# Optimization experiments

Hardware: AMD Instinct MI355X
Metric: run time of the kernel (lower is better)

## Reference

```python
import jax, jax.numpy as jnp
import numpy as np

B, T, D, H = 4, 2048, 1024, 8
d = D // H
EPS = 1e-12  # torch F.normalize eps


def _l2norm(x):
    n = jnp.sqrt(jnp.sum(x * x, axis=-1, keepdims=True))
    return x / jnp.maximum(n, EPS)


def setup_inputs() -> dict:
    key = jax.random.key(0)
    ks = jax.random.split(key, 7)
    s = 1.0 / np.sqrt(D)
    return {
        "x": jax.random.normal(ks[0], (B, T, D), dtype=jnp.float32),
        "Wq": jax.random.uniform(ks[1], (D, D), jnp.float32, -s, s),
        "Wk": jax.random.uniform(ks[2], (D, D), jnp.float32, -s, s),
        "Wv": jax.random.uniform(ks[3], (D, D), jnp.float32, -s, s),
        "Wo": jax.random.uniform(ks[4], (D, D), jnp.float32, -s, s),
        "Wlr": jax.random.uniform(ks[5], (D, D), jnp.float32, -s, s),
        "b_lr": jnp.zeros((D,), jnp.float32),
    }


def reference(x, Wq, Wk, Wv, Wo, Wlr, b_lr):
    # projections (torch Linear: y = x @ W.T)
    q = (x @ Wq.T).reshape(B, T, H, d)
    k = _l2norm((x @ Wk.T).reshape(B, T, H, d))
    v = _l2norm((x @ Wv.T).reshape(B, T, H, d))
    lr = jax.nn.sigmoid(x @ Wlr.T + b_lr).reshape(B, T, H, d)

    # scan over time; state w: [B,H,d,d]
    def step(w, qkvl):
        q_t, k_t, v_t, lr_t = qkvl  # each [B,H,d]
        v_old = jnp.einsum('bhij,bhj->bhi', w, k_t)          # retrieve
        w = w + (lr_t * (v_t - v_old))[..., :, None] * k_t[..., None, :]
        o_t = jnp.einsum('bhij,bhj->bhi', w, q_t)            # read
        return w, o_t

    to_t = lambda a: jnp.moveaxis(a, 1, 0)  # [B,T,H,d] -> [T,B,H,d]
    w0 = jnp.zeros((B, H, d, d), dtype=q.dtype)
    _, o = jax.lax.scan(step, w0, (to_t(q), to_t(k), to_t(v), to_t(lr)))
    o = jnp.moveaxis(o, 0, 1).reshape(B, T, D)
    return o @ Wo.T
```

## Files before the change

### kernel.cpp

```cpp
#include <hip/hip_runtime.h>
#include <math.h>

#define Bsz  4
#define Tlen 2048
#define Dm   1024
#define Hh   8
#define dh   128
#define Mrows (Bsz * Tlen)
#define CH   128
#define NCH  (Tlen / CH)

typedef __attribute__((ext_vector_type(8))) short  s16x8;
typedef __attribute__((ext_vector_type(4))) float  f32x4;

#define DPP_ADD(x, ctrl) \
    ((x) + __int_as_float(__builtin_amdgcn_update_dpp( \
        0, __float_as_int(x), (ctrl), 0xf, 0xf, true)))
#define SWZ_ADD16(x) \
    ((x) + __int_as_float(__builtin_amdgcn_ds_swizzle(__float_as_int(x), 0x401F)))

__device__ inline unsigned short f2b_rne(float f) {
    unsigned int u = __float_as_uint(f);
    u += 0x7FFFu + ((u >> 16) & 1u);
    return (unsigned short)(u >> 16);
}

__global__ __launch_bounds__(256) void cvt_f32_bf16(const float* __restrict__ in,
                                                    unsigned short* __restrict__ out)
{
    const size_t i = ((size_t)blockIdx.x * 256 + threadIdx.x) * 4;
    float4 v = *(const float4*)&in[i];
    ushort4 o;
    o.x = f2b_rne(v.x); o.y = f2b_rne(v.y);
    o.z = f2b_rne(v.z); o.w = f2b_rne(v.w);
    *(ushort4*)&out[i] = o;
}

__global__ __launch_bounds__(256) void gemm_bf16(const unsigned short* __restrict__ A,
                                                 const unsigned short* __restrict__ Wt,
                                                 const float* __restrict__ bias,
                                                 float* __restrict__ Yf,
                                                 unsigned short* __restrict__ Y16,
                                                 int mode)
{
    __shared__ __align__(16) unsigned short As[128 * 32];
    __shared__ __align__(16) unsigned short Bs[128 * 32];

    const int tid   = threadIdx.x;
    const int w     = tid >> 6;
    const int lane  = tid & 63;
    const int r4    = lane >> 2;
    const int p4    = lane & 3;
    const int row16 = lane & 15;
    const int quad  = lane >> 4;

    const int m0 = blockIdx.y * 128;
    const int n0 = blockIdx.x * 128;
    const int wm = (w >> 1) * 64;
    const int wn = (w & 1) * 64;

    f32x4 acc[4][4];
#pragma unroll
    for (int i = 0; i < 4; ++i)
#pragma unroll
        for (int j = 0; j < 4; ++j)
            acc[i][j] = (f32x4){0.f, 0.f, 0.f, 0.f};

    for (int k0 = 0; k0 < 1024; k0 += 32) {
        __syncthreads();
#pragma unroll
        for (int c = 0; c < 2; ++c) {
            const int ml  = w * 32 + c * 16 + r4;
            const int swz = (ml >> 1) & 3;
            const unsigned short* ga = A  + (size_t)(m0 + ml) * 1024 + k0 + ((p4 ^ swz) << 3);
            const unsigned short* gb = Wt + (size_t)(n0 + ml) * 1024 + k0 + ((p4 ^ swz) << 3);
            __builtin_amdgcn_global_load_lds(
                (const __attribute__((address_space(1))) void*)ga,
                (__attribute__((address_space(3))) void*)&As[(w * 32 + c * 16) * 32], 16, 0, 0);
            __builtin_amdgcn_global_load_lds(
                (const __attribute__((address_space(1))) void*)gb,
                (__attribute__((address_space(3))) void*)&Bs[(w * 32 + c * 16) * 32], 16, 0, 0);
        }
        __syncthreads();

        s16x8 af[4], bf[4];
#pragma unroll
        for (int bm = 0; bm < 4; ++bm) {
            const int ml  = wm + bm * 16 + row16;
            const int pos = quad ^ ((ml >> 1) & 3);
            af[bm] = *(const s16x8*)&As[ml * 32 + pos * 8];
        }
#pragma unroll
        for (int bn = 0; bn < 4; ++bn) {
            const int nl  = wn + bn * 16 + row16;
            const int pos = quad ^ ((nl >> 1) & 3);
            bf[bn] = *(const s16x8*)&Bs[nl * 32 + pos * 8];
        }
#pragma unroll
        for (int bm = 0; bm < 4; ++bm)
#pragma unroll
            for (int bn = 0; bn < 4; ++bn)
                acc[bm][bn] = __builtin_amdgcn_mfma_f32_16x16x32_bf16(af[bm], bf[bn], acc[bm][bn], 0, 0, 0);
    }

#pragma unroll
    for (int bm = 0; bm < 4; ++bm) {
        const int row = m0 + wm + bm * 16 + quad * 4;
#pragma unroll
        for (int bn = 0; bn < 4; ++bn) {
            const int col = n0 + wn + bn * 16 + row16;
            const float bb = bias ? bias[col] : 0.f;
#pragma unroll
            for (int r = 0; r < 4; ++r) {
                float val = acc[bm][bn][r] + bb;
                if (mode == 1) val = 1.f / (1.f + __expf(-val));
                if (mode == 2) Y16[(size_t)(row + r) * 1024 + col] = f2b_rne(val);
                else           Yf [(size_t)(row + r) * 1024 + col] = val;
            }
        }
    }
}

__global__ __launch_bounds__(256) void l2norm_rows(float* __restrict__ Kb,
                                                   float* __restrict__ Vb,
                                                   unsigned short* __restrict__ K16)
{
    const int gtid = blockIdx.x * 256 + threadIdx.x;
    const int row  = gtid >> 6;
    const int lane = threadIdx.x & 63;
    const size_t base = (size_t)row * dh + lane * 2;

    float2 k2 = *(float2*)&Kb[base];
    float2 v2 = *(float2*)&Vb[base];
    float sk = k2.x * k2.x + k2.y * k2.y;
    float sv = v2.x * v2.x + v2.y * v2.y;
#pragma unroll
    for (int off = 1; off < 64; off <<= 1) {
        sk += __shfl_xor(sk, off);
        sv += __shfl_xor(sv, off);
    }
    const float rk = 1.f / fmaxf(sqrtf(sk), 1e-12f);
    const float rv = 1.f / fmaxf(sqrtf(sv), 1e-12f);
    k2.x *= rk; k2.y *= rk;
    v2.x *= rv; v2.y *= rv;
    *(float2*)&Kb[base] = k2;
    *(float2*)&Vb[base] = v2;
    const unsigned int pk = (unsigned int)f2b_rne(k2.x) |
                            ((unsigned int)f2b_rne(k2.y) << 16);
    ((unsigned int*)K16)[base >> 1] = pk;
}

__global__ __launch_bounds__(64) void scan_coef(const float* __restrict__ Kb,
                                                const float* __restrict__ Vb,
                                                const float* __restrict__ LR,
                                                unsigned short* __restrict__ Ut,
                                                unsigned short* __restrict__ Wcp)
{
    const int bid = blockIdx.x;
    const int bh  = bid & 31;
    const int rg  = bid >> 5;
    const int b   = bh >> 3, h = bh & 7;
    const int lane = threadIdx.x;
    const int rl   = lane >> 5;
    const int c32  = lane & 31;
    const int row  = rg * 2 + rl;

    const size_t base = (size_t)b * Tlen * Dm + (size_t)h * dh;
    const float* kp = Kb + base + c32 * 4;
    const float* vp = Vb + base + row;
    const float* lp = LR + base + row;
    unsigned short* up = Ut + ((size_t)bh * dh + row) * Tlen;

    float w0 = 0.f, w1 = 0.f, w2 = 0.f, w3 = 0.f;

    float4 kr[8];
    float  vv[8], lv[8];
#pragma unroll
    for (int u = 0; u < 8; ++u) {
        const size_t off = (size_t)u * Dm;
        kr[u] = *(const float4*)(kp + off);
        vv[u] = vp[off];
        lv[u] = lp[off];
    }

    float o8[8];

    for (int t = 0; t < Tlen; t += 8) {
        if ((t & (CH - 1)) == 0) {
            const int c = t >> 7;
            uint2 wc;
            wc.x = (unsigned int)f2b_rne(w0) | ((unsigned int)f2b_rne(w1) << 16);
            wc.y = (unsigned int)f2b_rne(w2) | ((unsigned int)f2b_rne(w3) << 16);
            *(uint2*)&Wcp[(((size_t)bh * NCH + c) * dh + row) * dh + c32 * 4] = wc;
        }
#pragma unroll
        for (int u = 0; u < 8; ++u) {
            const int tc = t + u;
            const float4 k4 = kr[u];
            const float vr = vv[u], lrr = lv[u];

            int tn = tc + 8; if (tn >= Tlen) tn = Tlen - 1;
            const size_t offn = (size_t)tn * Dm;
            kr[u] = *(const float4*)(kp + offn);
            vv[u] = vp[offn];
            lv[u] = lp[offn];

            float d1 = fmaf(w1, k4.y, w0 * k4.x) + fmaf(w3, k4.w, w2 * k4.z);
            d1 = DPP_ADD(d1, 0xB1);
            d1 = DPP_ADD(d1, 0x4E);
            d1 = DPP_ADD(d1, 0x141);
            d1 = DPP_ADD(d1, 0x140);
            d1 = SWZ_ADD16(d1);

            const float coef = lrr * (vr - d1);
            w0 = fmaf(coef, k4.x, w0); w1 = fmaf(coef, k4.y, w1);
            w2 = fmaf(coef, k4.z, w2); w3 = fmaf(coef, k4.w, w3);
            o8[u] = coef;
        }
        uint4 pk;
        pk.x = (unsigned int)f2b_rne(o8[0]) | ((unsigned int)f2b_rne(o8[1]) << 16);
        pk.y = (unsigned int)f2b_rne(o8[2]) | ((unsigned int)f2b_rne(o8[3]) << 16);
        pk.z = (unsigned int)f2b_rne(o8[4]) | ((unsigned int)f2b_rne(o8[5]) << 16);
        pk.w = (unsigned int)f2b_rne(o8[6]) | ((unsigned int)f2b_rne(o8[7]) << 16);
        if (c32 == 0)
            *(uint4*)&up[t] = pk;
    }
}

__global__ __launch_bounds__(256) void chunk_o(const unsigned short* __restrict__ Q16,
                                               const unsigned short* __restrict__ K16,
                                               const unsigned short* __restrict__ Ut,
                                               const unsigned short* __restrict__ Wcp,
                                               unsigned short* __restrict__ Obb)
{
    __shared__ __align__(16) unsigned short As[128 * 32];
    __shared__ __align__(16) unsigned short Bs[128 * 32];
    __shared__ __align__(16) unsigned short Sb[128 * 136];

    const int blk = blockIdx.x;
    const int c   = blk & (NCH - 1);
    const int bh  = blk >> 4;
    const int b   = bh >> 3, h = bh & 7;

    const int tid   = threadIdx.x;
    const int w     = tid >> 6;
    const int lane  = tid & 63;
    const int r4    = lane >> 2;
    const int p4    = lane & 3;
    const int row16 = lane & 15;
    const int quad  = lane >> 4;
    const int wm = (w >> 1) * 64;
    const int wn = (w & 1) * 64;

    const size_t qkbase = (size_t)b * Tlen * Dm + (size_t)(c * CH) * Dm + (size_t)h * dh;
    const size_t ubase  = (size_t)bh * dh * Tlen + (size_t)c * CH;
    const size_t wbase  = ((size_t)bh * NCH + c) * dh * dh;

    f32x4 acc[4][4];
#pragma unroll
    for (int i = 0; i < 4; ++i)
#pragma unroll
        for (int j = 0; j < 4; ++j)
            acc[i][j] = (f32x4){0.f, 0.f, 0.f, 0.f};

    for (int k0 = 0; k0 < 128; k0 += 32) {
        __syncthreads();
#pragma unroll
        for (int cc = 0; cc < 2; ++cc) {
            const int ml  = w * 32 + cc * 16 + r4;
            const int swz = (ml >> 1) & 3;
            const unsigned short* ga = Q16 + qkbase + (size_t)ml * Dm + k0 + ((p4 ^ swz) << 3);
            const unsigned short* gb = K16 + qkbase + (size_t)ml * Dm + k0 + ((p4 ^ swz) << 3);
            __builtin_amdgcn_global_load_lds(
                (const __attribute__((address_space(1))) void*)ga,
                (__attribute__((address_space(3))) void*)&As[(w * 32 + cc * 16) * 32], 16, 0, 0);
            __builtin_amdgcn_global_load_lds(
                (const __attribute__((address_space(1))) void*)gb,
                (__attribute__((address_space(3))) void*)&Bs[(w * 32 + cc * 16) * 32], 16, 0, 0);
        }
        __syncthreads();

        s16x8 af[4], bf[4];
#pragma unroll
        for (int bm = 0; bm < 4; ++bm) {
            const int ml  = wm + bm * 16 + row16;
            const int pos = quad ^ ((ml >> 1) & 3);
            af[bm] = *(const s16x8*)&As[ml * 32 + pos * 8];
        }
#pragma unroll
        for (int bn = 0; bn < 4; ++bn) {
            const int nl  = wn + bn * 16 + row16;
            const int pos = quad ^ ((nl >> 1) & 3);
            bf[bn] = *(const s16x8*)&Bs[nl * 32 + pos * 8];
        }
#pragma unroll
        for (int bm = 0; bm < 4; ++bm)
#pragma unroll
            for (int bn = 0; bn < 4; ++bn)
                acc[bm][bn] = __builtin_amdgcn_mfma_f32_16x16x32_bf16(af[bm], bf[bn], acc[bm][bn], 0, 0, 0);
    }

#pragma unroll
    for (int bm = 0; bm < 4; ++bm) {
#pragma unroll
        for (int bn = 0; bn < 4; ++bn) {
            const int s_loc = wn + bn * 16 + row16;
#pragma unroll
            for (int r = 0; r < 4; ++r) {
                const int t_loc = wm + bm * 16 + quad * 4 + r;
                const float val = (s_loc <= t_loc) ? acc[bm][bn][r] : 0.f;
                Sb[t_loc * 136 + s_loc] = f2b_rne(val);
            }
            acc[bm][bn] = (f32x4){0.f, 0.f, 0.f, 0.f};
        }
    }

    for (int k0 = 0; k0 < 128; k0 += 32) {
        __syncthreads();
#pragma unroll
        for (int cc = 0; cc < 2; ++cc) {
            const int nl  = w * 32 + cc * 16 + r4;
            const int swz = (nl >> 1) & 3;
            const unsigned short* gb = Ut + ubase + (size_t)nl * Tlen + k0 + ((p4 ^ swz) << 3);
            __builtin_amdgcn_global_load_lds(
                (const __attribute__((address_space(1))) void*)gb,
                (__attribute__((address_space(3))) void*)&Bs[(w * 32 + cc * 16) * 32], 16, 0, 0);
        }
        __syncthreads();

        s16x8 af[4], bf[4];
#pragma unroll
        for (int bm = 0; bm < 4; ++bm) {
            const int ml = wm + bm * 16 + row16;
            af[bm] = *(const s16x8*)&Sb[ml * 136 + k0 + quad * 8];
        }
#pragma unroll
        for (int bn = 0; bn < 4; ++bn) {
            const int nl  = wn + bn * 16 + row16;
            const int pos = quad ^ ((nl >> 1) & 3);
            bf[bn] = *(const s16x8*)&Bs[nl * 32 + pos * 8];
        }
#pragma unroll
        for (int bm = 0; bm < 4; ++bm)
#pragma unroll
            for (int bn = 0; bn < 4; ++bn)
                acc[bm][bn] = __builtin_amdgcn_mfma_f32_16x16x32_bf16(af[bm], bf[bn], acc[bm][bn], 0, 0, 0);
    }

    for (int k0 = 0; k0 < 128; k0 += 32) {
        __syncthreads();
#pragma unroll
        for (int cc = 0; cc < 2; ++cc) {
            const int ml  = w * 32 + cc * 16 + r4;
            const int swz = (ml >> 1) & 3;
            const unsigned short* ga = Q16 + qkbase + (size_t)ml * Dm + k0 + ((p4 ^ swz) << 3);
            const unsigned short* gb = Wcp + wbase + (size_t)ml * dh + k0 + ((p4 ^ swz) << 3);
            __builtin_amdgcn_global_load_lds(
                (const __attribute__((address_space(1))) void*)ga,
                (__attribute__((address_space(3))) void*)&As[(w * 32 + cc * 16) * 32], 16, 0, 0);
            __builtin_amdgcn_global_load_lds(
                (const __attribute__((address_space(1))) void*)gb,
                (__attribute__((address_space(3))) void*)&Bs[(w * 32 + cc * 16) * 32], 16, 0, 0);
        }
        __syncthreads();

        s16x8 af[4], bf[4];
#pragma unroll
        for (int bm = 0; bm < 4; ++bm) {
            const int ml  = wm + bm * 16 + row16;
            const int pos = quad ^ ((ml >> 1) & 3);
            af[bm] = *(const s16x8*)&As[ml * 32 + pos * 8];
        }
#pragma unroll
        for (int bn = 0; bn < 4; ++bn) {
            const int nl  = wn + bn * 16 + row16;
            const int pos = quad ^ ((nl >> 1) & 3);
            bf[bn] = *(const s16x8*)&Bs[nl * 32 + pos * 8];
        }
#pragma unroll
        for (int bm = 0; bm < 4; ++bm)
#pragma unroll
            for (int bn = 0; bn < 4; ++bn)
                acc[bm][bn] = __builtin_amdgcn_mfma_f32_16x16x32_bf16(af[bm], bf[bn], acc[bm][bn], 0, 0, 0);
    }

#pragma unroll
    for (int bm = 0; bm < 4; ++bm) {
#pragma unroll
        for (int bn = 0; bn < 4; ++bn) {
            const int i_loc = wn + bn * 16 + row16;
#pragma unroll
            for (int r = 0; r < 4; ++r) {
                const int t_loc = wm + bm * 16 + quad * 4 + r;
                Obb[qkbase + (size_t)t_loc * Dm + i_loc] = f2b_rne(acc[bm][bn][r]);
            }
        }
    }
}

extern "C" void kernel_launch(void* const* d_in, const int* in_sizes, int n_in,
                              void* d_out, int out_size, void* d_ws, size_t ws_size,
                              hipStream_t stream)
{
    const float* x    = (const float*)d_in[0];
    const float* Wq   = (const float*)d_in[1];
    const float* Wk   = (const float*)d_in[2];
    const float* Wv   = (const float*)d_in[3];
    const float* Wo   = (const float*)d_in[4];
    const float* Wlr  = (const float*)d_in[5];
    const float* b_lr = (const float*)d_in[6];

    float* ws = (float*)d_ws;
    const size_t S  = (size_t)Mrows * Dm;
    const size_t SW = (size_t)Dm * Dm;
    float* Kb  = ws;
    float* Vb  = ws + S;
    float* LRb = ws + 2 * S;
    unsigned short* xb   = (unsigned short*)(ws + 3 * S);
    unsigned short* Wcp  = xb;
    unsigned short* Q16  = xb + S;
    unsigned short* K16  = Q16 + S;
    unsigned short* Ut   = K16 + S;
    unsigned short* Obb  = Ut + S;
    unsigned short* Wqb  = Obb + S;
    unsigned short* Wkb  = Wqb + SW;
    unsigned short* Wvb  = Wkb + SW;
    unsigned short* Wlrb = Wvb + SW;
    unsigned short* Wob  = Wlrb + SW;

    cvt_f32_bf16<<<S / 1024, 256, 0, stream>>>(x, xb);
    cvt_f32_bf16<<<SW / 1024, 256, 0, stream>>>(Wq, Wqb);
    cvt_f32_bf16<<<SW / 1024, 256, 0, stream>>>(Wk, Wkb);
    cvt_f32_bf16<<<SW / 1024, 256, 0, stream>>>(Wv, Wvb);
    cvt_f32_bf16<<<SW / 1024, 256, 0, stream>>>(Wlr, Wlrb);
    cvt_f32_bf16<<<SW / 1024, 256, 0, stream>>>(Wo, Wob);

    dim3 gg(Dm / 128, Mrows / 128);
    gemm_bf16<<<gg, 256, 0, stream>>>(xb, Wqb, nullptr, nullptr, Q16, 2);
    gemm_bf16<<<gg, 256, 0, stream>>>(xb, Wkb, nullptr, Kb, nullptr, 0);
    gemm_bf16<<<gg, 256, 0, stream>>>(xb, Wvb, nullptr, Vb, nullptr, 0);
    gemm_bf16<<<gg, 256, 0, stream>>>(xb, Wlrb, b_lr, LRb, nullptr, 1);

    l2norm_rows<<<(Bsz * Tlen * Hh) / 4, 256, 0, stream>>>(Kb, Vb, K16);

    scan_coef<<<Bsz * Hh * 64, 64, 0, stream>>>(Kb, Vb, LRb, Ut, Wcp);

    chunk_o<<<Bsz * Hh * NCH, 256, 0, stream>>>(Q16, K16, Ut, Wcp, Obb);

    gemm_bf16<<<gg, 256, 0, stream>>>(Obb, Wob, nullptr, (float*)d_out, nullptr, 0);
}
```

Measured before the change: 639.9 us.

## Replace sequential delta-rule scan with chunked Gram-matrix solve on MFMA

Replaces the per-timestep serial scan with a chunked formulation over chunks of 64 steps. A new kernel computes the per-chunk key Gram matrix and transposed key tiles, using split hi/lo bf16 for extra precision. One workgroup per batch-head then solves the in-chunk triangular system for the update coefficients and updates the 128x128 state with MFMA. This removes the long chain of 2048 dependent steps, each doing a cross-lane reduction, in exchange for extra matrix work and a kernel with only 32 workgroups and a large LDS footprint.

```diff
diff --git a/kernel.cpp b/kernel.cpp
--- a/kernel.cpp
+++ b/kernel.cpp
@@ -9,20 +9,20 @@
 #define Mrows (Bsz * Tlen)
 #define CH   128
 #define NCH  (Tlen / CH)
+#define C64  64
+#define NC64 (Tlen / C64)
 
 typedef __attribute__((ext_vector_type(8))) short  s16x8;
 typedef __attribute__((ext_vector_type(4))) float  f32x4;
-
-#define DPP_ADD(x, ctrl) \
-    ((x) + __int_as_float(__builtin_amdgcn_update_dpp( \
-        0, __float_as_int(x), (ctrl), 0xf, 0xf, true)))
-#define SWZ_ADD16(x) \
-    ((x) + __int_as_float(__builtin_amdgcn_ds_swizzle(__float_as_int(x), 0x401F)))
+typedef __attribute__((ext_vector_type(2))) float  f32x2;
 
 __device__ inline unsigned short f2b_rne(float f) {
     unsigned int u = __float_as_uint(f);
     u += 0x7FFFu + ((u >> 16) & 1u);
     return (unsigned short)(u >> 16);
+}
+__device__ inline float b2f(unsigned short u) {
+    return __uint_as_float(((unsigned int)u) << 16);
 }
 
 __global__ __launch_bounds__(256) void cvt_f32_bf16(const float* __restrict__ in,
@@ -123,7 +123,8 @@
 
 __global__ __launch_bounds__(256) void l2norm_rows(float* __restrict__ Kb,
                                                    float* __restrict__ Vb,
-                                                   unsigned short* __restrict__ K16)
+                                                   unsigned short* __restrict__ K16,
+                                                   unsigned short* __restrict__ K16lo)
 {
     const int gtid = blockIdx.x * 256 + threadIdx.x;
     const int row  = gtid >> 6;
@@ -145,85 +146,337 @@
     v2.x *= rv; v2.y *= rv;
     *(float2*)&Kb[base] = k2;
     *(float2*)&Vb[base] = v2;
-    const unsigned int pk = (unsigned int)f2b_rne(k2.x) |
-                            ((unsigned int)f2b_rne(k2.y) << 16);
-    ((unsigned int*)K16)[base >> 1] = pk;
-}
-
-__global__ __launch_bounds__(64) void scan_coef(const float* __restrict__ Kb,
-                                                const float* __restrict__ Vb,
-                                                const float* __restrict__ LR,
-                                                unsigned short* __restrict__ Ut,
-                                                unsigned short* __restrict__ Wcp)
+    const unsigned short hx = f2b_rne(k2.x), hy = f2b_rne(k2.y);
+    ((unsigned int*)K16)[base >> 1] = (unsigned int)hx | ((unsigned int)hy << 16);
+    const unsigned short lx = f2b_rne(k2.x - b2f(hx));
+    const unsigned short ly = f2b_rne(k2.y - b2f(hy));
+    ((unsigned int*)K16lo)[base >> 1] = (unsigned int)lx | ((unsigned int)ly << 16);
+}
+
+__global__ __launch_bounds__(256) void gram_kt(const unsigned short* __restrict__ K16,
+                                               const unsigned short* __restrict__ K16lo,
+                                               float* __restrict__ Gf,
+                                               unsigned short* __restrict__ KThi,
+                                               unsigned short* __restrict__ KTlo)
 {
-    const int bid = blockIdx.x;
-    const int bh  = bid & 31;
-    const int rg  = bid >> 5;
+    __shared__ __align__(16) unsigned short Kp[2][64 * 136];
+
+    const int blk = blockIdx.x;
+    const int c   = blk & 31;
+    const int bh  = blk >> 5;
     const int b   = bh >> 3, h = bh & 7;
-    const int lane = threadIdx.x;
-    const int rl   = lane >> 5;
-    const int c32  = lane & 31;
-    const int row  = rg * 2 + rl;
-
-    const size_t base = (size_t)b * Tlen * Dm + (size_t)h * dh;
-    const float* kp = Kb + base + c32 * 4;
-    const float* vp = Vb + base + row;
-    const float* lp = LR + base + row;
-    unsigned short* up = Ut + ((size_t)bh * dh + row) * Tlen;
-
-    float w0 = 0.f, w1 = 0.f, w2 = 0.f, w3 = 0.f;
-
-    float4 kr[8];
-    float  vv[8], lv[8];
-#pragma unroll
-    for (int u = 0; u < 8; ++u) {
-        const size_t off = (size_t)u * Dm;
-        kr[u] = *(const float4*)(kp + off);
-        vv[u] = vp[off];
-        lv[u] = lp[off];
-    }
-
-    float o8[8];
-
-    for (int t = 0; t < Tlen; t += 8) {
-        if ((t & (CH - 1)) == 0) {
-            const int c = t >> 7;
-            uint2 wc;
-            wc.x = (unsigned int)f2b_rne(w0) | ((unsigned int)f2b_rne(w1) << 16);
-            wc.y = (unsigned int)f2b_rne(w2) | ((unsigned int)f2b_rne(w3) << 16);
-            *(uint2*)&Wcp[(((size_t)bh * NCH + c) * dh + row) * dh + c32 * 4] = wc;
-        }
-#pragma unroll
-        for (int u = 0; u < 8; ++u) {
-            const int tc = t + u;
-            const float4 k4 = kr[u];
-            const float vr = vv[u], lrr = lv[u];
-
-            int tn = tc + 8; if (tn >= Tlen) tn = Tlen - 1;
-            const size_t offn = (size_t)tn * Dm;
-            kr[u] = *(const float4*)(kp + offn);
-            vv[u] = vp[offn];
-            lv[u] = lp[offn];
-
-            float d1 = fmaf(w1, k4.y, w0 * k4.x) + fmaf(w3, k4.w, w2 * k4.z);
-            d1 = DPP_ADD(d1, 0xB1);
-            d1 = DPP_ADD(d1, 0x4E);
-            d1 = DPP_ADD(d1, 0x141);
-            d1 = DPP_ADD(d1, 0x140);
-            d1 = SWZ_ADD16(d1);
-
-            const float coef = lrr * (vr - d1);
-            w0 = fmaf(coef, k4.x, w0); w1 = fmaf(coef, k4.y, w1);
-            w2 = fmaf(coef, k4.z, w2); w3 = fmaf(coef, k4.w, w3);
-            o8[u] = coef;
-        }
-        uint4 pk;
-        pk.x = (unsigned int)f2b_rne(o8[0]) | ((unsigned int)f2b_rne(o8[1]) << 16);
-        pk.y = (unsigned int)f2b_rne(o8[2]) | ((unsigned int)f2b_rne(o8[3]) << 16);
-        pk.z = (unsigned int)f2b_rne(o8[4]) | ((unsigned int)f2b_rne(o8[5]) << 16);
-        pk.w = (unsigned int)f2b_rne(o8[6]) | ((unsigned int)f2b_rne(o8[7]) << 16);
-        if (c32 == 0)
-            *(uint4*)&up[t] = pk;
+    const int tid = threadIdx.x;
+
+    {
+        const int row = tid >> 2, seg = (tid & 3) * 32;
+        const size_t gsrc = ((size_t)(b * Tlen + c * C64 + row)) * Dm + h * dh + seg;
+        const s16x8* ph = (const s16x8*)&K16[gsrc];
+        const s16x8* pl = (const s16x8*)&K16lo[gsrc];
+#pragma unroll
+        for (int q = 0; q < 4; ++q) {
+            *(s16x8*)&Kp[0][row * 136 + seg + q * 8] = ph[q];
+            *(s16x8*)&Kp[1][row * 136 + seg + q * 8] = pl[q];
+        }
+    }
+    __syncthreads();
+
+    const int w     = tid >> 6;
+    const int lane  = tid & 63;
+    const int row16 = lane & 15;
+    const int quad  = lane >> 4;
+    const int sh = (w >> 1) * 32;
+    const int th = (w & 1) * 32;
+
+    f32x4 ag[2][2];
+#pragma unroll
+    for (int i = 0; i < 2; ++i)
+#pragma unroll
+        for (int j = 0; j < 2; ++j)
+            ag[2 > i ? i : i][j] = (f32x4){0.f, 0.f, 0.f, 0.f};
+
+#pragma unroll
+    for (int pass = 0; pass < 3; ++pass) {
+        const int pa = (pass == 2) ? 1 : 0;
+        const int pb = (pass == 1) ? 1 : 0;
+#pragma unroll
+        for (int k0 = 0; k0 < 128; k0 += 32) {
+            s16x8 af[2], bf[2];
+#pragma unroll
+            for (int bm = 0; bm < 2; ++bm) {
+                const int ml = sh + bm * 16 + row16;
+                af[bm] = *(const s16x8*)&Kp[pa][ml * 136 + k0 + quad * 8];
+            }
+#pragma unroll
+            for (int bn = 0; bn < 2; ++bn) {
+                const int nl = th + bn * 16 + row16;
+                bf[bn] = *(const s16x8*)&Kp[pb][nl * 136 + k0 + quad * 8];
+            }
+#pragma unroll
+            for (int bm = 0; bm < 2; ++bm)
+#pragma unroll
+                for (int bn = 0; bn < 2; ++bn)
+                    ag[bm][bn] = __builtin_amdgcn_mfma_f32_16x16x32_bf16(af[bm], bf[bn], ag[bm][bn], 0, 0, 0);
+        }
+    }
+
+    float* gout = Gf + ((size_t)(bh * 32 + c)) * 4096;
+#pragma unroll
+    for (int bm = 0; bm < 2; ++bm)
+#pragma unroll
+        for (int bn = 0; bn < 2; ++bn) {
+            const int t = th + bn * 16 + row16;
+#pragma unroll
+            for (int r = 0; r < 4; ++r) {
+                const int s = sh + bm * 16 + quad * 4 + r;
+                gout[s * 64 + t] = ag[bm][bn][r];
+            }
+        }
+
+    {
+        const int j   = tid >> 1;
+        const int th2 = (tid & 1) * 32;
+        unsigned int pk[16];
+#pragma unroll
+        for (int hl = 0; hl < 2; ++hl) {
+#pragma unroll
+            for (int p = 0; p < 16; ++p) {
+                const unsigned short e0 = Kp[hl][(th2 + 2 * p) * 136 + j];
+                const unsigned short e1 = Kp[hl][(th2 + 2 * p + 1) * 136 + j];
+                pk[p] = (unsigned int)e0 | ((unsigned int)e1 << 16);
+            }
+            unsigned short* dst = (hl ? KTlo : KThi) +
+                ((size_t)(bh * 32 + c) * 128 + j) * 64 + th2;
+#pragma unroll
+            for (int q = 0; q < 4; ++q)
+                *(uint4*)&dst[q * 8] = *(uint4*)&pk[q * 4];
+        }
+    }
+}
+
+__global__ __launch_bounds__(256) void solve_coef(const unsigned short* __restrict__ K16,
+                                                  const float* __restrict__ Vb,
+                                                  const float* __restrict__ LRb,
+                                                  const float* __restrict__ Gf,
+                                                  const unsigned short* __restrict__ KThi,
+                                                  const unsigned short* __restrict__ KTlo,
+                                                  unsigned short* __restrict__ Ut,
+                                                  unsigned short* __restrict__ Wcp)
+{
+    extern __shared__ __align__(16) char smem[];
+    unsigned short* Khs = (unsigned short*)smem;
+    unsigned short* Ws  = (unsigned short*)(smem + 16384);
+    float*          Gs  = (float*)(smem + 49152);
+    unsigned short* Uhi = (unsigned short*)(smem + 65536);
+    unsigned short* Ulo = (unsigned short*)(smem + 81920);
+
+    const int bh = blockIdx.x;
+    const int b  = bh >> 3, h = bh & 7;
+    const int tid   = threadIdx.x;
+    const int w     = tid >> 6;
+    const int lane  = tid & 63;
+    const int p4    = lane & 3;
+    const int row16 = lane & 15;
+    const int quad  = lane >> 4;
+    const int wm = (w >> 1) * 64;
+    const int wn = (w & 1) * 64;
+    const int ih  = (w >> 1) * 64;
+    const int th2 = (w & 1) * 32;
+
+    f32x4 Wa[4][4];
+#pragma unroll
+    for (int i = 0; i < 4; ++i)
+#pragma unroll
+        for (int j = 0; j < 4; ++j)
+            Wa[i][j] = (f32x4){0.f, 0.f, 0.f, 0.f};
+
+    const int ilane = w * 64 + lane;
+    f32x2 r2[32];
+
+#pragma unroll 1
+    for (int c = 0; c < NC64; ++c) {
+        const int t0g = c * C64;
+
+#pragma unroll
+        for (int c4 = 0; c4 < 4; ++c4) {
+            const int rr = c4 * 16 + (lane >> 2);
+            const unsigned short* ga = K16 + ((size_t)(b * Tlen + t0g + rr)) * Dm + h * dh
+                                       + w * 32 + ((p4 ^ ((rr >> 1) & 3)) << 3);
+            __builtin_amdgcn_global_load_lds(
+                (const __attribute__((address_space(1))) void*)ga,
+                (__attribute__((address_space(3))) void*)((char*)Khs + w * 4096 + c4 * 1024 + lane * 16),
+                16, 0, 0);
+        }
+        {
+            const size_t gbase = (size_t)(bh * 32 + c) * 4096;
+#pragma unroll
+            for (int c4 = 0; c4 < 4; ++c4) {
+                const float* gg = Gf + gbase + w * 1024 + c4 * 256 + lane * 4;
+                __builtin_amdgcn_global_load_lds(
+                    (const __attribute__((address_space(1))) void*)gg,
+                    (__attribute__((address_space(3))) void*)((char*)Gs + (w * 1024 + c4 * 256 + lane * 4) * 4),
+                    16, 0, 0);
+            }
+        }
+#pragma unroll
+        for (int bm = 0; bm < 4; ++bm)
+#pragma unroll
+            for (int bn = 0; bn < 4; ++bn) {
+                const int j  = wn + bn * 16 + row16;
+                const int sl = j >> 5, jj = j & 31;
+#pragma unroll
+                for (int r = 0; r < 4; ++r) {
+                    const int i = wm + bm * 16 + quad * 4 + r;
+                    Ws[sl * 4096 + i * 32 + (((jj >> 3) ^ ((i >> 1) & 3)) << 3) + (j & 7)] =
+                        f2b_rne(Wa[bm][bn][r]);
+                }
+            }
+        __syncthreads();
+
+        {
+            f32x4 aA[4][2];
+#pragma unroll
+            for (int i = 0; i < 4; ++i)
+#pragma unroll
+                for (int j = 0; j < 2; ++j)
+                    aA[i][j] = (f32x4){0.f, 0.f, 0.f, 0.f};
+#pragma unroll
+            for (int k0s = 0; k0s < 4; ++k0s) {
+                s16x8 af[4], bf[2];
+#pragma unroll
+                for (int bm = 0; bm < 4; ++bm) {
+                    const int ml = ih + bm * 16 + row16;
+                    af[bm] = *(const s16x8*)&Ws[k0s * 4096 + ml * 32 + ((quad ^ ((ml >> 1) & 3)) << 3)];
+                }
+#pragma unroll
+                for (int bn = 0; bn < 2; ++bn) {
+                    const int nl = th2 + bn * 16 + row16;
+                    bf[bn] = *(const s16x8*)&Khs[k0s * 2048 + nl * 32 + ((quad ^ ((nl >> 1) & 3)) << 3)];
+                }
+#pragma unroll
+                for (int bm = 0; bm < 4; ++bm)
+#pragma unroll
+                    for (int bn = 0; bn < 2; ++bn)
+                        aA[bm][bn] = __builtin_amdgcn_mfma_f32_16x16x32_bf16(af[bm], bf[bn], aA[bm][bn], 0, 0, 0);
+            }
+#pragma unroll
+            for (int bm = 0; bm < 4; ++bm)
+#pragma unroll
+                for (int bn = 0; bn < 2; ++bn) {
+                    const int t = th2 + bn * 16 + row16;
+#pragma unroll
+                    for (int r = 0; r < 4; ++r) {
+                        const int i = ih + bm * 16 + quad * 4 + r;
+                        Ulo[t * 128 + (((i >> 3) ^ (t & 7)) << 3) + (i & 7)] = f2b_rne(aA[bm][bn][r]);
+                    }
+                }
+        }
+        if ((c & 1) == 0) {
+            const int i2 = tid >> 1, half = tid & 1;
+            unsigned short* dstrow = Wcp + ((size_t)(bh * NCH + (c >> 1)) * 128 + i2) * 128;
+#pragma unroll
+            for (int sl = 0; sl < 4; ++sl)
+#pragma unroll
+                for (int gq = 0; gq < 2; ++gq) {
+                    const int gg = half * 2 + gq;
+                    s16x8 v = *(const s16x8*)&Ws[sl * 4096 + i2 * 32 + ((gg ^ ((i2 >> 1) & 3)) << 3)];
+                    *(s16x8*)&dstrow[sl * 32 + gg * 8] = v;
+                }
+        }
+        __syncthreads();
+
+        if (w >= 2) {
+            const int base2 = (w - 2) * 2;
+#pragma unroll
+            for (int bb = 0; bb < 2; ++bb) {
+                const int buf = base2 + bb;
+                const int st  = buf & 1;
+                const unsigned short* src = (buf < 2) ? KThi : KTlo;
+#pragma unroll
+                for (int c8 = 0; c8 < 8; ++c8) {
+                    const int jj = c8 * 16 + (lane >> 2);
+                    const unsigned short* ga = src + ((size_t)(bh * 32 + c) * 128 + jj) * 64
+                                               + st * 32 + ((p4 ^ ((jj >> 1) & 3)) << 3);
+                    __builtin_amdgcn_global_load_lds(
+                        (const __attribute__((address_space(1))) void*)ga,
+                        (__attribute__((address_space(3))) void*)((char*)Ws + buf * 8192 + c8 * 1024 + lane * 16),
+                        16, 0, 0);
+                }
+            }
+        } else {
+            const int i = ilane;
+            const float* vp  = Vb  + ((size_t)(b * Tlen + t0g)) * Dm + h * dh + i;
+            const float* lrp = LRb + ((size_t)(b * Tlen + t0g)) * Dm + h * dh + i;
+#pragma unroll
+            for (int p = 0; p < 32; ++p) {
+                const int ta = 2 * p, tb = 2 * p + 1;
+                const float a0a = b2f(Ulo[ta * 128 + (((i >> 3) ^ (ta & 7)) << 3) + (i & 7)]);
+                const float a0b = b2f(Ulo[tb * 128 + (((i >> 3) ^ (tb & 7)) << 3) + (i & 7)]);
+                r2[p].x = vp[(size_t)ta * Dm] - a0a;
+                r2[p].y = vp[(size_t)tb * Dm] - a0b;
+            }
+            float lv[8], o8[8];
+#pragma unroll
+            for (int s = 0; s < C64; ++s) {
+                if ((s & 7) == 0) {
+#pragma unroll
+                    for (int u = 0; u < 8; ++u)
+                        lv[u] = lrp[(size_t)(s + u) * Dm];
+                }
+                const float rs = (s & 1) ? r2[s >> 1].y : r2[s >> 1].x;
+                const float cf = lv[s & 7] * rs;
+                o8[s & 7] = cf;
+                const f32x2 cf2 = (f32x2){cf, cf};
+#pragma unroll
+                for (int p = (s + 1) >> 1; p < 32; ++p) {
+                    const f32x2 gg = *(const f32x2*)&Gs[s * 64 + 2 * p];
+                    r2[p] -= cf2 * gg;
+                }
+                if ((s & 7) == 7) {
+                    const int t0 = s - 7;
+                    unsigned int phi[4], plo[4];
+#pragma unroll
+                    for (int q = 0; q < 4; ++q) {
+                        const unsigned short h0 = f2b_rne(o8[2 * q]);
+                        const unsigned short h1 = f2b_rne(o8[2 * q + 1]);
+                        const unsigned short l0 = f2b_rne(o8[2 * q] - b2f(h0));
+                        const unsigned short l1 = f2b_rne(o8[2 * q + 1] - b2f(h1));
+                        phi[q] = (unsigned int)h0 | ((unsigned int)h1 << 16);
+                        plo[q] = (unsigned int)l0 | ((unsigned int)l1 << 16);
+                    }
+                    const int lg  = (t0 >> 3) ^ (i & 7);
+                    *(uint4*)&Uhi[i * 64 + (lg << 3)] = *(uint4*)phi;
+                    *(uint4*)&Ulo[i * 64 + (lg << 3)] = *(uint4*)plo;
+                    *(uint4*)&Ut[(size_t)(bh * 128 + i) * Tlen + t0g + t0] = *(uint4*)phi;
+                }
+            }
+        }
+        __syncthreads();
+
+#pragma unroll
+        for (int pass = 0; pass < 3; ++pass) {
+            const unsigned short* Ua = (pass == 1) ? Ulo : Uhi;
+            const int bufbase = (pass == 2) ? 2 : 0;
+#pragma unroll
+            for (int st = 0; st < 2; ++st) {
+                s16x8 af[4], bf[4];
+#pragma unroll
+                for (int bm = 0; bm < 4; ++bm) {
+                    const int ml = wm + bm * 16 + row16;
+                    af[bm] = *(const s16x8*)&Ua[ml * 64 + (((st * 4 + quad) ^ (ml & 7)) << 3)];
+                }
+#pragma unroll
+                for (int bn = 0; bn < 4; ++bn) {
+                    const int nl = wn + bn * 16 + row16;
+                    bf[bn] = *(const s16x8*)&Ws[(bufbase + st) * 4096 + nl * 32 + ((quad ^ ((nl >> 1) & 3)) << 3)];
+                }
+#pragma unroll
+                for (int bm = 0; bm < 4; ++bm)
+#pragma unroll
+                    for (int bn = 0; bn < 4; ++bn)
+                        Wa[bm][bn] = __builtin_amdgcn_mfma_f32_16x16x32_bf16(af[bm], bf[bn], Wa[bm][bn], 0, 0, 0);
+            }
+        }
+        __syncthreads();
     }
 }
 
@@ -427,6 +680,17 @@
     unsigned short* Wvb  = Wkb + SW;
     unsigned short* Wlrb = Wvb + SW;
     unsigned short* Wob  = Wlrb + SW;
+    unsigned short* K16lo = Ut;
+    float*          Gf    = (float*)Obb;
+    unsigned short* KThi  = (unsigned short*)Kb;
+    unsigned short* KTlo  = KThi + S;
+
+    static int attr_done = 0;
+    if (!attr_done) {
+        (void)hipFuncSetAttribute((const void*)solve_coef,
+                                  hipFuncAttributeMaxDynamicSharedMemorySize, 98304);
+        attr_done = 1;
+    }
 
     cvt_f32_bf16<<<S / 1024, 256, 0, stream>>>(x, xb);
     cvt_f32_bf16<<<SW / 1024, 256, 0, stream>>>(Wq, Wqb);
@@ -441,9 +705,11 @@
     gemm_bf16<<<gg, 256, 0, stream>>>(xb, Wvb, nullptr, Vb, nullptr, 0);
     gemm_bf16<<<gg, 256, 0, stream>>>(xb, Wlrb, b_lr, LRb, nullptr, 1);
 
-    l2norm_rows<<<(Bsz * Tlen * Hh) / 4, 256, 0, stream>>>(Kb, Vb, K16);
-
-    scan_coef<<<Bsz * Hh * 64, 64, 0, stream>>>(Kb, Vb, LRb, Ut, Wcp);
+    l2norm_rows<<<(Bsz * Tlen * Hh) / 4, 256, 0, stream>>>(Kb, Vb, K16, K16lo);
+
+    gram_kt<<<32 * 32, 256, 0, stream>>>(K16, K16lo, Gf, KThi, KTlo);
+
+    solve_coef<<<32, 256, 98304, stream>>>(K16, Vb, LRb, Gf, KThi, KTlo, Ut, Wcp);
 
     chunk_o<<<Bsz * Hh * NCH, 256, 0, stream>>>(Q16, K16, Ut, Wcp, Obb);
 
```

Result: slower. 732.5 us (+14.5%).
